# Kernel optimization log

Hardware: AMD Instinct MI355X
Metric: run time of the kernel (lower is better)

The kernel has to match this reference:

```python
import jax, jax.numpy as jnp
import numpy as np

B = 16          # graphs per batch
NN = 2000       # nodes per graph (num_nodes)
N = B * NN      # total nodes in the batched graph
F_IN = 128      # input node features
H, C = 4, 64    # heads, per-head out channels (both GAT layers)
HC = H * C
DEG = 12        # average degree per node
FC1, FC2, OUT = 512, 128, 1
FC_IN = 6 * NN  # len(which_layer) = 6


def setup_inputs() -> dict:
    key = jax.random.key(0)
    ks = jax.random.split(key, 32)

    def g(i, shape, s=0.05):
        return jax.random.normal(ks[i], shape, jnp.float32) * s

    # within-graph random edges, no self loops (GATConv removes then re-adds them)
    src_l = jax.random.randint(ks[0], (B, NN * DEG), 0, NN)
    off = jax.random.randint(ks[1], (B, NN * DEG), 1, NN)
    dst_l = (src_l + off) % NN
    goff = (jnp.arange(B) * NN)[:, None]
    edge_index = jnp.stack([(src_l + goff).reshape(-1),
                            (dst_l + goff).reshape(-1)]).astype(jnp.int32)

    return {
        "x": g(2, (N, F_IN), 1.0),
        "W1": g(3, (F_IN, HC)), "att_src1": g(4, (H, C)), "att_dst1": g(5, (H, C)),
        "b1": jnp.zeros((HC,), jnp.float32),
        "W2": g(6, (HC, HC)), "att_src2": g(7, (H, C)), "att_dst2": g(8, (H, C)),
        "b2": jnp.zeros((HC,), jnp.float32),
        "pw1": g(9, (HC, 1)), "pb1": jnp.zeros((1,), jnp.float32),
        "pw2": g(10, (HC, 1)), "pb2": jnp.zeros((1,), jnp.float32),
        "ln_w": jnp.ones((NN,), jnp.float32), "ln_b": jnp.zeros((NN,), jnp.float32),
        "sex_emb": g(11, (2, NN)), "mut_emb": g(12, (4, NN)),
        "age_w": g(13, (NN,)), "age_b": jnp.zeros((NN,), jnp.float32),
        "fw1": g(14, (FC_IN, FC1)), "fb1": jnp.zeros((FC1,), jnp.float32),
        "fw2": g(15, (FC1, FC2)), "fb2": jnp.zeros((FC2,), jnp.float32),
        "fw3": g(16, (FC2, OUT)), "fb3": jnp.zeros((OUT,), jnp.float32),
        "age": jax.random.uniform(ks[17], (B,), jnp.float32),
        "edge_index": edge_index,
        "sex": jax.random.randint(ks[18], (B,), 0, 2),
        "mutation": jax.random.randint(ks[19], (B,), 0, 4),
    }


def _layer_norm(x, w, b, eps=1e-5):
    mu = jnp.mean(x, -1, keepdims=True)
    var = jnp.mean((x - mu) ** 2, -1, keepdims=True)
    return (x - mu) / jnp.sqrt(var + eps) * w + b


def _gat_conv(x, W, att_src, att_dst, bias, src, dst):
    h = (x @ W).reshape(N, H, C)                         # [N,H,C]
    a_s = jnp.sum(h * att_src[None], -1)                 # [N,H]
    a_d = jnp.sum(h * att_dst[None], -1)                 # [N,H]
    alpha = jax.nn.leaky_relu(a_s[src] + a_d[dst], 0.2)  # [E,H]
    m = jax.ops.segment_max(alpha, dst, num_segments=N)  # segment softmax over dst
    e = jnp.exp(alpha - m[dst])
    denom = jax.ops.segment_sum(e, dst, num_segments=N)
    a = e / (denom[dst] + 1e-16)
    out = jax.ops.segment_sum(a[:, :, None] * h[src], dst, num_segments=N)
    return out.reshape(N, HC) + bias


def _forward(x, W1, att_src1, att_dst1, b1, W2, att_src2, att_dst2, b2,
             pw1, pb1, pw2, pb2, ln_w, ln_b, sex_emb, mut_emb, age_w, age_b,
             fw1, fb1, fw2, fb2, fw3, fb3, age, edge_index, sex, mutation):
    loop = jnp.arange(N, dtype=edge_index.dtype)         # self loops added by GATConv
    src = jnp.concatenate([edge_index[0], loop])
    dst = jnp.concatenate([edge_index[1], loop])

    x0 = jnp.mean(x, -1).reshape(B, NN)                  # to_dense_batch(mean(x,-1))

    h = jax.nn.relu(_gat_conv(x, W1, att_src1, att_dst1, b1, src, dst))
    x1 = (h @ pw1 + pb1).squeeze(-1).reshape(B, NN)
    h = jax.nn.relu(_gat_conv(h, W2, att_src2, att_dst2, b2, src, dst))
    x2 = (h @ pw2 + pb2).squeeze(-1).reshape(B, NN)

    x0 = _layer_norm(x0, ln_w, ln_b)
    x1 = _layer_norm(x1, ln_w, ln_b)
    x2 = _layer_norm(x2, ln_w, ln_b)
    ms = jnp.concatenate([x0, x1, x2], axis=1)           # [B, 3*NN]

    demo = jnp.concatenate([sex_emb[sex], mut_emb[mutation],
                            age[:, None] * age_w[None, :] + age_b], axis=1)
    t = jnp.concatenate([demo, ms], axis=1)              # [B, 6*NN]
    t = jax.nn.relu(t @ fw1 + fb1)
    t = jax.nn.relu(t @ fw2 + fb2)
    pred = t @ fw3 + fb3                                 # [B, 1]
    return pred, x0, x1, x2, ms


def reference(x, W1, att_src1, att_dst1, b1, W2, att_src2, att_dst2, b2,
              pw1, pb1, pw2, pb2, ln_w, ln_b, sex_emb, mut_emb, age_w, age_b,
              fw1, fb1, fw2, fb2, fw3, fb3, age, edge_index, sex, mutation):
    return _forward(x, W1, att_src1, att_dst1, b1, W2, att_src2, att_dst2, b2,
                    pw1, pb1, pw2, pb2, ln_w, ln_b, sex_emb, mut_emb, age_w, age_b,
                    fw1, fb1, fw2, fb2, fw3, fb3, age, edge_index, sex, mutation)
```

## Files before the change

kernel.cpp:

```cpp
#include <hip/hip_runtime.h>
#include <math.h>

#define NTOT   32000
#define NNODE  2000
#define NB     16
#define FIN    128
#define HCDIM  256
#define NH     4
#define FC1DIM 512
#define FC2DIM 128
#define FCIN   12000
#define NCH    125
#define KCC    96
#define CAP    64
#define BK     32
#define LPITCH 40
#define TRB    384
#define DEMOB  375

typedef __attribute__((ext_vector_type(8))) short bf16x8;
typedef __attribute__((ext_vector_type(4))) float f32x4;

__device__ inline float4 ld4(const float* p){ return *reinterpret_cast<const float4*>(p); }
__device__ inline void st4(float* p, float4 v){ *reinterpret_cast<float4*>(p) = v; }
__device__ inline float4 add4(float4 a, float4 b){ return make_float4(a.x+b.x,a.y+b.y,a.z+b.z,a.w+b.w); }
__device__ inline float lrelu(float x){ return x > 0.f ? x : 0.2f*x; }
__device__ inline float4 leaky4(float4 a){ return make_float4(lrelu(a.x),lrelu(a.y),lrelu(a.z),lrelu(a.w)); }
__device__ inline float4 exp4u(float4 a){ return make_float4(__expf(a.x),__expf(a.y),__expf(a.z),__expf(a.w)); }
__device__ inline float dot4(float4 a, float4 b){ return a.x*b.x + a.y*b.y + a.z*b.z + a.w*b.w; }
__device__ inline float selh(float4 v, int h){ return h==0 ? v.x : (h==1 ? v.y : (h==2 ? v.z : v.w)); }

__device__ inline unsigned short f2bf(float f){
  unsigned int u = __float_as_uint(f);
  u += 0x7FFFu + ((u >> 16) & 1u);
  return (unsigned short)(u >> 16);
}
__device__ inline unsigned int pk2bf(float a, float b){
  return (unsigned int)f2bf(a) | ((unsigned int)f2bf(b) << 16);
}
__device__ inline float bf2f(unsigned short h){
  return __uint_as_float(((unsigned int)h) << 16);
}
__device__ inline float4 ldbf4(const unsigned short* p){
  ushort4 v = *reinterpret_cast<const ushort4*>(p);
  return make_float4(bf2f(v.x), bf2f(v.y), bf2f(v.z), bf2f(v.w));
}

__global__ __launch_bounds__(256) void k_zero(int* __restrict__ cnt){
  int i = blockIdx.x*256 + threadIdx.x;
  if(i < NTOT) cnt[i] = 0;
}

__device__ __forceinline__ void ln_impl(const float* __restrict__ src,
                                        const float* __restrict__ lnw,
                                        const float* __restrict__ lnb,
                                        float* __restrict__ o1,
                                        float* __restrict__ o2,
                                        float* __restrict__ o3,
                                        float* red){
  int tid = threadIdx.x, lane = tid & 63, wv = tid >> 6;
  float s = 0.f, ss = 0.f;
  for(int i = tid; i < NNODE; i += 256){ float v = src[i]; s += v; ss += v*v; }
  #pragma unroll
  for(int off=1; off<64; off<<=1){ s += __shfl_xor(s, off); ss += __shfl_xor(ss, off); }
  if(lane == 0){ red[wv] = s; red[4+wv] = ss; }
  __syncthreads();
  s  = red[0]+red[1]+red[2]+red[3];
  ss = red[4]+red[5]+red[6]+red[7];
  float mu  = s * (1.0f/NNODE);
  float var = ss * (1.0f/NNODE) - mu*mu;
  float inv = 1.0f / sqrtf(var + 1e-5f);
  for(int i = tid; i < NNODE; i += 256){
    float v = (src[i]-mu)*inv*lnw[i] + lnb[i];
    o1[i] = v; o2[i] = v; o3[i] = v;
  }
}

__global__ void k_misc(const int* __restrict__ src, const int* __restrict__ dst,
                       int* __restrict__ cnt, int* __restrict__ col, int e0, int eb,
                       const float* __restrict__ W1, const float* __restrict__ W2,
                       unsigned short* __restrict__ W1t, unsigned short* __restrict__ W2t,
                       const float* __restrict__ sexemb, const float* __restrict__ mutemb,
                       const float* __restrict__ agew, const float* __restrict__ ageb,
                       const float* __restrict__ age, const int* __restrict__ sex,
                       const int* __restrict__ mut, float* __restrict__ t,
                       const float* __restrict__ x, float* __restrict__ x0r){
  int blk = blockIdx.x;
  if(blk < eb){
    int i = blk*256 + threadIdx.x;
    if(i < e0){
      int d = dst[i];
      int slot = atomicAdd(&cnt[d], 1);
      if(slot < CAP) col[(d<<6) + slot] = src[i];
    }
  } else if(blk < eb + TRB){
    int idx = (blk - eb)*256 + threadIdx.x;
    if(idx < HCDIM*FIN){
      int n = idx / FIN, k = idx - n*FIN;
      W1t[idx] = f2bf(W1[(size_t)k*HCDIM + n]);
    } else {
      int j = idx - HCDIM*FIN;
      int n = j / HCDIM, k = j - n*HCDIM;
      W2t[j] = f2bf(W2[(size_t)k*HCDIM + n]);
    }
  } else if(blk < eb + TRB + DEMOB){
    int i = (blk - eb - TRB)*256 + threadIdx.x;
    int b = i / (3*NNODE);
    int j = i - b*(3*NNODE);
    float v;
    if(j < NNODE)          v = sexemb[sex[b]*NNODE + j];
    else if(j < 2*NNODE)   v = mutemb[mut[b]*NNODE + (j - NNODE)];
    else                   v = age[b]*agew[j - 2*NNODE] + ageb[j - 2*NNODE];
    t[b*FCIN + j] = v;
  } else {
    int lane = threadIdx.x & 63, wv = threadIdx.x >> 6;
    int n = (blk - eb - TRB - DEMOB)*4 + wv;
    const float* r = x + (size_t)n*FIN;
    float2 v = *reinterpret_cast<const float2*>(r + lane*2);
    float s = v.x + v.y;
    #pragma unroll
    for(int off=1; off<64; off<<=1) s += __shfl_xor(s, off);
    if(lane == 0) x0r[n] = s * (1.0f/FIN);
  }
}

template<int AF32>
__global__ __launch_bounds__(256) void k_gemm_bf(const void* __restrict__ Av,
                                                 const unsigned short* __restrict__ Bt,
                                                 unsigned short* __restrict__ C,
                                                 const float* __restrict__ attS,
                                                 const float* __restrict__ attD,
                                                 float* __restrict__ a_s,
                                                 float* __restrict__ a_d,
                                                 int M, int K){
  const unsigned short* A = (const unsigned short*)Av;
  const float*         Af = (const float*)Av;
  __shared__ unsigned short As[128][LPITCH];
  __shared__ unsigned short Bs[128][LPITCH];
  int tid = threadIdx.x;
  int lane = tid & 63, wv = tid >> 6;
  int wm = (wv & 1)*64, wn = (wv >> 1)*64;
  int m0 = blockIdx.y*128, n0 = blockIdx.x*128;
  int l15 = lane & 15, lq = lane >> 4;
  f32x4 acc[4][4];
  #pragma unroll
  for(int i=0;i<4;i++)
    #pragma unroll
    for(int j=0;j<4;j++)
      acc[i][j] = (f32x4){0.f,0.f,0.f,0.f};

  int r = tid >> 2, c = (tid & 3)*8;
  for(int k0 = 0; k0 < K; k0 += BK){
    if(AF32){
      const float* pa  = Af + (size_t)(m0+r)*K + k0 + c;
      const float* pa2 = Af + (size_t)(m0+r+64)*K + k0 + c;
      float4 u0 = ld4(pa),  u1 = ld4(pa+4);
      float4 v0 = ld4(pa2), v1 = ld4(pa2+4);
      uint4 w0, w1;
      w0.x = pk2bf(u0.x,u0.y); w0.y = pk2bf(u0.z,u0.w);
      w0.z = pk2bf(u1.x,u1.y); w0.w = pk2bf(u1.z,u1.w);
      w1.x = pk2bf(v0.x,v0.y); w1.y = pk2bf(v0.z,v0.w);
      w1.z = pk2bf(v1.x,v1.y); w1.w = pk2bf(v1.z,v1.w);
      *reinterpret_cast<uint4*>(&As[r][c])    = w0;
      *reinterpret_cast<uint4*>(&As[r+64][c]) = w1;
    } else {
      *reinterpret_cast<uint4*>(&As[r][c])    = *reinterpret_cast<const uint4*>(A  + (size_t)(m0+r)*K + k0 + c);
      *reinterpret_cast<uint4*>(&As[r+64][c]) = *reinterpret_cast<const uint4*>(A  + (size_t)(m0+r+64)*K + k0 + c);
    }
    *reinterpret_cast<uint4*>(&Bs[r][c])    = *reinterpret_cast<const uint4*>(Bt + (size_t)(n0+r)*K + k0 + c);
    *reinterpret_cast<uint4*>(&Bs[r+64][c]) = *reinterpret_cast<const uint4*>(Bt + (size_t)(n0+r+64)*K + k0 + c);
    __syncthreads();
    bf16x8 af[4], bfr[4];
    #pragma unroll
    for(int i=0;i<4;i++){
      af[i]  = *reinterpret_cast<const bf16x8*>(&As[wm + i*16 + l15][lq*8]);
      bfr[i] = *reinterpret_cast<const bf16x8*>(&Bs[wn + i*16 + l15][lq*8]);
    }
    #pragma unroll
    for(int mi=0;mi<4;mi++)
      #pragma unroll
      for(int ni=0;ni<4;ni++)
        acc[mi][ni] = __builtin_amdgcn_mfma_f32_16x16x32_bf16(af[mi], bfr[ni], acc[mi][ni], 0, 0, 0);
    __syncthreads();
  }
  #pragma unroll
  for(int mi=0;mi<4;mi++){
    #pragma unroll
    for(int ni=0;ni<4;ni++){
      int cn = n0 + wn + ni*16 + l15;
      #pragma unroll
      for(int rg=0;rg<4;rg++){
        int rm = m0 + wm + mi*16 + lq*4 + rg;
        C[(size_t)rm*HCDIM + cn] = f2bf(acc[mi][ni][rg]);
      }
    }
  }
  int head = (n0 + wn) >> 6;
  float avs[4], avd[4];
  #pragma unroll
  for(int ni=0;ni<4;ni++){
    int cc = ni*16 + l15;
    avs[ni] = attS[head*64 + cc];
    avd[ni] = attD[head*64 + cc];
  }
  #pragma unroll
  for(int mi=0;mi<4;mi++){
    #pragma unroll
    for(int rg=0;rg<4;rg++){
      float ps = 0.f, pd = 0.f;
      #pragma unroll
      for(int ni=0;ni<4;ni++){
        float v = acc[mi][ni][rg];
        ps = fmaf(avs[ni], v, ps);
        pd = fmaf(avd[ni], v, pd);
      }
      #pragma unroll
      for(int off=1; off<16; off<<=1){
        ps += __shfl_xor(ps, off);
        pd += __shfl_xor(pd, off);
      }
      if(l15 == 0){
        int rm = m0 + wm + mi*16 + lq*4 + rg;
        a_s[rm*4 + head] = ps;
        a_d[rm*4 + head] = pd;
      }
    }
  }
}

template<int STORE>
__global__ __launch_bounds__(256) void k_agg(const unsigned short* __restrict__ hpre,
                                             const float* __restrict__ a_s,
                                             const float* __restrict__ a_d,
                                             const int* __restrict__ cnt,
                                             const int* __restrict__ col,
                                             const float* __restrict__ bias,
                                             const float* __restrict__ pw,
                                             const float* __restrict__ pb,
                                             unsigned short* __restrict__ hout,
                                             float* __restrict__ xraw,
                                             const float* __restrict__ lnsrc,
                                             const float* __restrict__ lnw,
                                             const float* __restrict__ lnb,
                                             float* __restrict__ out,
                                             float* __restrict__ t,
                                             int which){
  __shared__ float4 ew[4][CAP];
  __shared__ int    cols[4][CAP];
  __shared__ float  lred[8];
  int bx = blockIdx.x;
  if(bx < 16){
    int b = bx;
    ln_impl(lnsrc + b*NNODE, lnw, lnb,
            out + 16 + which*(NB*NNODE) + b*NNODE,
            out + 16 + 3*(NB*NNODE) + b*(3*NNODE) + which*NNODE,
            t + b*FCIN + 3*NNODE + which*NNODE, lred);
    return;
  }
  int tid = threadIdx.x;
  int lane = tid & 63, wv = tid >> 6;
  int blk  = bx - 16;
  int xcd  = blk & 7;
  int slot = blk >> 3;
  int half = slot / 500;
  int g    = xcd + 8*half;
  int n    = g*NNODE + (slot - half*500)*4 + wv;
  int f0 = lane*4;
  int hl = lane >> 4;
  float4 ad   = ld4(a_d + n*4);
  float4 asn  = ld4(a_s + n*4);
  float4 eself = exp4u(leaky4(add4(asn, ad)));
  int deg = min(cnt[n], CAP);
  int base = n << 6;
  if(lane < deg){
    int s = col[base + lane];
    cols[wv][lane] = s;
    ew[wv][lane] = exp4u(leaky4(add4(ld4(a_s + s*4), ad)));
  }
  float es = selh(eself, hl);
  float dsum = es;
  float4 hv = ldbf4(hpre + (size_t)n*HCDIM + f0);
  float4 acc = make_float4(es*hv.x, es*hv.y, es*hv.z, es*hv.w);
  const float* ewf = (const float*)&ew[wv][0];
  const int*   cwf = &cols[wv][0];
  for(int e = 0; e < deg; e++){
    int s = cwf[e];
    float w = ewf[e*4 + hl];
    dsum += w;
    float4 h2 = ldbf4(hpre + (size_t)s*HCDIM + f0);
    acc.x = fmaf(w, h2.x, acc.x); acc.y = fmaf(w, h2.y, acc.y);
    acc.z = fmaf(w, h2.z, acc.z); acc.w = fmaf(w, h2.w, acc.w);
  }
  float invh = 1.0f / (dsum + 1e-16f);
  float4 b4 = ld4(bias + f0);
  acc = make_float4(fmaxf(fmaf(acc.x,invh,b4.x),0.f), fmaxf(fmaf(acc.y,invh,b4.y),0.f),
                    fmaxf(fmaf(acc.z,invh,b4.z),0.f), fmaxf(fmaf(acc.w,invh,b4.w),0.f));
  if(STORE){
    ushort4 hb = make_ushort4(f2bf(acc.x), f2bf(acc.y), f2bf(acc.z), f2bf(acc.w));
    *reinterpret_cast<ushort4*>(hout + (size_t)n*HCDIM + f0) = hb;
  }
  float part = dot4(acc, ld4(pw + f0));
  #pragma unroll
  for(int off=1; off<64; off<<=1) part += __shfl_xor(part, off);
  if(lane == 0) xraw[n] = part + pb[0];
}

__global__ __launch_bounds__(256) void k_lnx2(const float* __restrict__ x2r,
                                              const float* __restrict__ lnw,
                                              const float* __restrict__ lnb,
                                              float* __restrict__ out,
                                              float* __restrict__ t){
  __shared__ float red[8];
  int b = blockIdx.x;
  ln_impl(x2r + b*NNODE, lnw, lnb,
          out + 16 + 2*(NB*NNODE) + b*NNODE,
          out + 16 + 3*(NB*NNODE) + b*(3*NNODE) + 2*NNODE,
          t + b*FCIN + 3*NNODE + 2*NNODE, red);
}

__global__ __launch_bounds__(256) void k_fc1(const float* __restrict__ t,
                                             const float* __restrict__ fw1,
                                             float* __restrict__ partial){
  __shared__ float ts[NB][KCC];
  int blk = blockIdx.x;
  int chunk = blk >> 1;
  int halfc = blk & 1;
  int tid = threadIdx.x;
  int k0 = chunk * KCC;
  #pragma unroll
  for(int i = tid; i < NB*KCC; i += 256){
    int b = i / KCC, kk = i - b*KCC;
    ts[b][kk] = t[b*FCIN + k0 + kk];
  }
  __syncthreads();
  int j = halfc*256 + tid;
  float acc[NB];
  #pragma unroll
  for(int b=0;b<NB;b++) acc[b] = 0.f;
  const float* wp = fw1 + (size_t)k0*FC1DIM + j;
  #pragma unroll 4
  for(int kk = 0; kk < KCC; kk++){
    float w = wp[(size_t)kk*FC1DIM];
    #pragma unroll
    for(int b=0;b<NB;b++) acc[b] = fmaf(ts[b][kk], w, acc[b]);
  }
  float* po = partial + (size_t)chunk*(NB*FC1DIM) + j;
  #pragma unroll
  for(int b=0;b<NB;b++) po[b*FC1DIM] = acc[b];
}

__global__ __launch_bounds__(256) void k_head(const float* __restrict__ partial,
                                              const float* __restrict__ fb1,
                                              const float* __restrict__ fw2,
                                              const float* __restrict__ fb2,
                                              const float* __restrict__ fw3,
                                              const float* __restrict__ fb3,
                                              float* __restrict__ pred){
  __shared__ float t1s[FC1DIM];
  __shared__ float red[2];
  int b = blockIdx.x, tid = threadIdx.x;
  int e1 = tid, e2 = tid + 256;
  float s1 = fb1[e1], s2 = fb1[e2];
  const float* pb_ = partial + (size_t)b*FC1DIM;
  for(int c = 0; c < NCH; c++){
    const float* pc = pb_ + (size_t)c*(NB*FC1DIM);
    s1 += pc[e1];
    s2 += pc[e2];
  }
  t1s[e1] = fmaxf(s1, 0.f);
  t1s[e2] = fmaxf(s2, 0.f);
  __syncthreads();
  if(tid < FC2DIM){
    int j = tid;
    float s = fb2[j];
    for(int k = 0; k < FC1DIM; k++) s = fmaf(t1s[k], fw2[k*FC2DIM + j], s);
    s = fmaxf(s, 0.f) * fw3[j];
    #pragma unroll
    for(int off=1; off<64; off<<=1) s += __shfl_xor(s, off);
    int lane = j & 63, wv = j >> 6;
    if(lane == 0) red[wv] = s;
  }
  __syncthreads();
  if(tid == 0) pred[b] = red[0] + red[1] + fb3[0];
}

extern "C" void kernel_launch(void* const* d_in, const int* in_sizes, int n_in,
                              void* d_out, int out_size, void* d_ws, size_t ws_size,
                              hipStream_t stream) {
  const float* x       = (const float*)d_in[0];
  const float* W1      = (const float*)d_in[1];
  const float* attS1   = (const float*)d_in[2];
  const float* attD1   = (const float*)d_in[3];
  const float* b1      = (const float*)d_in[4];
  const float* W2      = (const float*)d_in[5];
  const float* attS2   = (const float*)d_in[6];
  const float* attD2   = (const float*)d_in[7];
  const float* b2      = (const float*)d_in[8];
  const float* pw1     = (const float*)d_in[9];
  const float* pb1     = (const float*)d_in[10];
  const float* pw2     = (const float*)d_in[11];
  const float* pb2     = (const float*)d_in[12];
  const float* lnw     = (const float*)d_in[13];
  const float* lnb     = (const float*)d_in[14];
  const float* sexemb  = (const float*)d_in[15];
  const float* mutemb  = (const float*)d_in[16];
  const float* agew    = (const float*)d_in[17];
  const float* ageb    = (const float*)d_in[18];
  const float* fw1     = (const float*)d_in[19];
  const float* fb1     = (const float*)d_in[20];
  const float* fw2     = (const float*)d_in[21];
  const float* fb2     = (const float*)d_in[22];
  const float* fw3     = (const float*)d_in[23];
  const float* fb3     = (const float*)d_in[24];
  const float* age     = (const float*)d_in[25];
  const int*   eidx    = (const int*)d_in[26];
  const int*   sex     = (const int*)d_in[27];
  const int*   mut     = (const int*)d_in[28];
  const int E0 = in_sizes[26] / 2;
  const int* esrc = eidx;
  const int* edst = eidx + E0;

  float* out = (float*)d_out;

  float* w = (float*)d_ws;
  float* a_s  = w;
  float* a_d  = a_s + NTOT*NH;
  float* x0r  = a_d + NTOT*NH;
  float* x1r  = x0r + NTOT;
  float* x2r  = x1r + NTOT;
  float* tbuf = x2r + NTOT;
  float* part = tbuf + NB*FCIN;
  float* t1   = part + (size_t)240*NB*FC1DIM;
  unsigned short* hA  = (unsigned short*)(t1 + NB*FC1DIM);
  unsigned short* hB  = hA  + (size_t)NTOT*HCDIM;
  unsigned short* W1t = hB  + (size_t)NTOT*HCDIM;
  unsigned short* W2t = W1t + HCDIM*FIN;
  int* cnt    = (int*)(W2t + HCDIM*HCDIM);
  int* col    = cnt + NTOT;
  (void)ws_size; (void)n_in; (void)out_size;

  const int eb = (E0 + 255)/256;

  k_zero<<<(NTOT+255)/256, 256, 0, stream>>>(cnt);
  k_misc<<<eb + TRB + DEMOB + NTOT/4, 256, 0, stream>>>(esrc, edst, cnt, col, E0, eb,
                                               W1, W2, W1t, W2t,
                                               sexemb, mutemb, agew, ageb,
                                               age, sex, mut, tbuf, x, x0r);

  k_gemm_bf<1><<<dim3(HCDIM/128, NTOT/128), 256, 0, stream>>>(x, W1t, hA, attS1, attD1, a_s, a_d, NTOT, FIN);
  k_agg<1><<<16 + NTOT/4, 256, 0, stream>>>(hA, a_s, a_d, cnt, col, b1, pw1, pb1, hB, x1r,
                                            x0r, lnw, lnb, out, tbuf, 0);

  k_gemm_bf<0><<<dim3(HCDIM/128, NTOT/128), 256, 0, stream>>>(hB, W2t, hA, attS2, attD2, a_s, a_d, NTOT, HCDIM);
  k_agg<0><<<16 + NTOT/4, 256, 0, stream>>>(hA, a_s, a_d, cnt, col, b2, pw2, pb2, hB, x2r,
                                            x1r, lnw, lnb, out, tbuf, 1);

  k_lnx2<<<NB, 256, 0, stream>>>(x2r, lnw, lnb, out, tbuf);

  k_fc1<<<NCH*2, 256, 0, stream>>>(tbuf, fw1, part);
  k_head<<<NB, 256, 0, stream>>>(part, fb1, fw2, fb2, fw3, fb3, out);
}
```

Before: 276.3 us.

## Fuse x0 row-mean into GEMM, tile weight transpose, prefetch agg gathers, split FC

Moves the per-node input mean computation into the first GEMM's A-tile load so x is read once, and removes those blocks from the misc kernel. Replaces the scalar strided weight transpose with LDS-tiled 64x64 transposes for coalesced access. In the aggregation loop, the next neighbour's feature row is prefetched one step ahead using a sentinel column. Doubles the FC1 chunk count with smaller chunks and splits the FC2 dot over all 256 threads in the head kernel. These trade extra partial buffers and registers for better parallelism and less memory latency.

```diff
diff --git a/kernel.cpp b/kernel.cpp
--- a/kernel.cpp
+++ b/kernel.cpp
@@ -10,12 +10,12 @@
 #define FC1DIM 512
 #define FC2DIM 128
 #define FCIN   12000
-#define NCH    125
-#define KCC    96
+#define NCH    250
+#define KCC    48
 #define CAP    64
 #define BK     32
 #define LPITCH 40
-#define TRB    384
+#define TRB2   24
 #define DEMOB  375
 
 typedef __attribute__((ext_vector_type(8))) short bf16x8;
@@ -83,8 +83,8 @@
                        const float* __restrict__ sexemb, const float* __restrict__ mutemb,
                        const float* __restrict__ agew, const float* __restrict__ ageb,
                        const float* __restrict__ age, const int* __restrict__ sex,
-                       const int* __restrict__ mut, float* __restrict__ t,
-                       const float* __restrict__ x, float* __restrict__ x0r){
+                       const int* __restrict__ mut, float* __restrict__ t){
+  __shared__ float tile[64][65];
   int blk = blockIdx.x;
   if(blk < eb){
     int i = blk*256 + threadIdx.x;
@@ -93,18 +93,41 @@
       int slot = atomicAdd(&cnt[d], 1);
       if(slot < CAP) col[(d<<6) + slot] = src[i];
     }
-  } else if(blk < eb + TRB){
-    int idx = (blk - eb)*256 + threadIdx.x;
-    if(idx < HCDIM*FIN){
-      int n = idx / FIN, k = idx - n*FIN;
-      W1t[idx] = f2bf(W1[(size_t)k*HCDIM + n]);
+  } else if(blk < eb + TRB2){
+    int tb = blk - eb;
+    int wv = threadIdx.x >> 6, lane = threadIdx.x & 63;
+    if(tb < 8){
+      int tk = tb >> 2, tn = tb & 3;
+      int k0 = tk*64, n0 = tn*64;
+      #pragma unroll
+      for(int q=0;q<16;q++){
+        int row = q*4 + wv;
+        tile[row][lane] = W1[(size_t)(k0+row)*HCDIM + n0 + lane];
+      }
+      __syncthreads();
+      #pragma unroll
+      for(int q=0;q<16;q++){
+        int row = q*4 + wv;
+        W1t[(size_t)(n0+row)*FIN + k0 + lane] = f2bf(tile[lane][row]);
+      }
     } else {
-      int j = idx - HCDIM*FIN;
-      int n = j / HCDIM, k = j - n*HCDIM;
-      W2t[j] = f2bf(W2[(size_t)k*HCDIM + n]);
-    }
-  } else if(blk < eb + TRB + DEMOB){
-    int i = (blk - eb - TRB)*256 + threadIdx.x;
+      int t2 = tb - 8;
+      int tk = t2 >> 2, tn = t2 & 3;
+      int k0 = tk*64, n0 = tn*64;
+      #pragma unroll
+      for(int q=0;q<16;q++){
+        int row = q*4 + wv;
+        tile[row][lane] = W2[(size_t)(k0+row)*HCDIM + n0 + lane];
+      }
+      __syncthreads();
+      #pragma unroll
+      for(int q=0;q<16;q++){
+        int row = q*4 + wv;
+        W2t[(size_t)(n0+row)*HCDIM + k0 + lane] = f2bf(tile[lane][row]);
+      }
+    }
+  } else {
+    int i = (blk - eb - TRB2)*256 + threadIdx.x;
     int b = i / (3*NNODE);
     int j = i - b*(3*NNODE);
     float v;
@@ -112,15 +135,6 @@
     else if(j < 2*NNODE)   v = mutemb[mut[b]*NNODE + (j - NNODE)];
     else                   v = age[b]*agew[j - 2*NNODE] + ageb[j - 2*NNODE];
     t[b*FCIN + j] = v;
-  } else {
-    int lane = threadIdx.x & 63, wv = threadIdx.x >> 6;
-    int n = (blk - eb - TRB - DEMOB)*4 + wv;
-    const float* r = x + (size_t)n*FIN;
-    float2 v = *reinterpret_cast<const float2*>(r + lane*2);
-    float s = v.x + v.y;
-    #pragma unroll
-    for(int off=1; off<64; off<<=1) s += __shfl_xor(s, off);
-    if(lane == 0) x0r[n] = s * (1.0f/FIN);
   }
 }
 
@@ -132,6 +146,7 @@
                                                  const float* __restrict__ attD,
                                                  float* __restrict__ a_s,
                                                  float* __restrict__ a_d,
+                                                 float* __restrict__ x0r,
                                                  int M, int K){
   const unsigned short* A = (const unsigned short*)Av;
   const float*         Af = (const float*)Av;
@@ -150,12 +165,15 @@
       acc[i][j] = (f32x4){0.f,0.f,0.f,0.f};
 
   int r = tid >> 2, c = (tid & 3)*8;
+  float rs1 = 0.f, rs2 = 0.f;
   for(int k0 = 0; k0 < K; k0 += BK){
     if(AF32){
       const float* pa  = Af + (size_t)(m0+r)*K + k0 + c;
       const float* pa2 = Af + (size_t)(m0+r+64)*K + k0 + c;
       float4 u0 = ld4(pa),  u1 = ld4(pa+4);
       float4 v0 = ld4(pa2), v1 = ld4(pa2+4);
+      rs1 += (u0.x+u0.y+u0.z+u0.w) + (u1.x+u1.y+u1.z+u1.w);
+      rs2 += (v0.x+v0.y+v0.z+v0.w) + (v1.x+v1.y+v1.z+v1.w);
       uint4 w0, w1;
       w0.x = pk2bf(u0.x,u0.y); w0.y = pk2bf(u0.z,u0.w);
       w0.z = pk2bf(u1.x,u1.y); w0.w = pk2bf(u1.z,u1.w);
@@ -182,6 +200,15 @@
       for(int ni=0;ni<4;ni++)
         acc[mi][ni] = __builtin_amdgcn_mfma_f32_16x16x32_bf16(af[mi], bfr[ni], acc[mi][ni], 0, 0, 0);
     __syncthreads();
+  }
+  if(AF32 && n0 == 0){
+    float s1 = rs1, s2 = rs2;
+    s1 += __shfl_xor(s1,1); s1 += __shfl_xor(s1,2);
+    s2 += __shfl_xor(s2,1); s2 += __shfl_xor(s2,2);
+    if((tid & 3) == 0){
+      x0r[m0 + r]      = s1 * (1.0f/FIN);
+      x0r[m0 + r + 64] = s2 * (1.0f/FIN);
+    }
   }
   #pragma unroll
   for(int mi=0;mi<4;mi++){
@@ -246,7 +273,7 @@
                                              float* __restrict__ t,
                                              int which){
   __shared__ float4 ew[4][CAP];
-  __shared__ int    cols[4][CAP];
+  __shared__ int    cols[4][CAP+1];
   __shared__ float  lred[8];
   int bx = blockIdx.x;
   if(bx < 16){
@@ -276,20 +303,25 @@
     int s = col[base + lane];
     cols[wv][lane] = s;
     ew[wv][lane] = exp4u(leaky4(add4(ld4(a_s + s*4), ad)));
-  }
+  } else {
+    cols[wv][lane] = n;
+  }
+  if(lane == 0) cols[wv][CAP] = n;
   float es = selh(eself, hl);
   float dsum = es;
   float4 hv = ldbf4(hpre + (size_t)n*HCDIM + f0);
   float4 acc = make_float4(es*hv.x, es*hv.y, es*hv.z, es*hv.w);
   const float* ewf = (const float*)&ew[wv][0];
   const int*   cwf = &cols[wv][0];
+  float4 h2 = ldbf4(hpre + (size_t)cwf[0]*HCDIM + f0);
   for(int e = 0; e < deg; e++){
-    int s = cwf[e];
+    int sn = cwf[e+1];
+    float4 hn = ldbf4(hpre + (size_t)sn*HCDIM + f0);
     float w = ewf[e*4 + hl];
     dsum += w;
-    float4 h2 = ldbf4(hpre + (size_t)s*HCDIM + f0);
     acc.x = fmaf(w, h2.x, acc.x); acc.y = fmaf(w, h2.y, acc.y);
     acc.z = fmaf(w, h2.z, acc.z); acc.w = fmaf(w, h2.w, acc.w);
+    h2 = hn;
   }
   float invh = 1.0f / (dsum + 1e-16f);
   float4 b4 = ld4(bias + f0);
@@ -327,7 +359,6 @@
   int halfc = blk & 1;
   int tid = threadIdx.x;
   int k0 = chunk * KCC;
-  #pragma unroll
   for(int i = tid; i < NB*KCC; i += 256){
     int b = i / KCC, kk = i - b*KCC;
     ts[b][kk] = t[b*FCIN + k0 + kk];
@@ -338,7 +369,7 @@
   #pragma unroll
   for(int b=0;b<NB;b++) acc[b] = 0.f;
   const float* wp = fw1 + (size_t)k0*FC1DIM + j;
-  #pragma unroll 4
+  #pragma unroll 8
   for(int kk = 0; kk < KCC; kk++){
     float w = wp[(size_t)kk*FC1DIM];
     #pragma unroll
@@ -357,11 +388,13 @@
                                               const float* __restrict__ fb3,
                                               float* __restrict__ pred){
   __shared__ float t1s[FC1DIM];
+  __shared__ float ph[128];
   __shared__ float red[2];
   int b = blockIdx.x, tid = threadIdx.x;
   int e1 = tid, e2 = tid + 256;
   float s1 = fb1[e1], s2 = fb1[e2];
   const float* pb_ = partial + (size_t)b*FC1DIM;
+  #pragma unroll 4
   for(int c = 0; c < NCH; c++){
     const float* pc = pb_ + (size_t)c*(NB*FC1DIM);
     s1 += pc[e1];
@@ -370,15 +403,20 @@
   t1s[e1] = fmaxf(s1, 0.f);
   t1s[e2] = fmaxf(s2, 0.f);
   __syncthreads();
-  if(tid < FC2DIM){
-    int j = tid;
-    float s = fb2[j];
-    for(int k = 0; k < FC1DIM; k++) s = fmaf(t1s[k], fw2[k*FC2DIM + j], s);
+  int j = tid & 127, hc = tid >> 7;
+  float s = (hc == 0) ? fb2[j] : 0.f;
+  const float* w2 = fw2 + (size_t)(hc*256)*FC2DIM + j;
+  #pragma unroll 4
+  for(int k = 0; k < 256; k++) s = fmaf(t1s[hc*256 + k], w2[(size_t)k*FC2DIM], s);
+  if(hc == 1) ph[j] = s;
+  __syncthreads();
+  if(hc == 0){
+    s += ph[j];
     s = fmaxf(s, 0.f) * fw3[j];
     #pragma unroll
     for(int off=1; off<64; off<<=1) s += __shfl_xor(s, off);
-    int lane = j & 63, wv = j >> 6;
-    if(lane == 0) red[wv] = s;
+    int lane = j & 63, wv2 = j >> 6;
+    if(lane == 0) red[wv2] = s;
   }
   __syncthreads();
   if(tid == 0) pred[b] = red[0] + red[1] + fb3[0];
@@ -430,7 +468,7 @@
   float* x2r  = x1r + NTOT;
   float* tbuf = x2r + NTOT;
   float* part = tbuf + NB*FCIN;
-  float* t1   = part + (size_t)240*NB*FC1DIM;
+  float* t1   = part + (size_t)256*NB*FC1DIM;
   unsigned short* hA  = (unsigned short*)(t1 + NB*FC1DIM);
   unsigned short* hB  = hA  + (size_t)NTOT*HCDIM;
   unsigned short* W1t = hB  + (size_t)NTOT*HCDIM;
@@ -442,16 +480,16 @@
   const int eb = (E0 + 255)/256;
 
   k_zero<<<(NTOT+255)/256, 256, 0, stream>>>(cnt);
-  k_misc<<<eb + TRB + DEMOB + NTOT/4, 256, 0, stream>>>(esrc, edst, cnt, col, E0, eb,
+  k_misc<<<eb + TRB2 + DEMOB, 256, 0, stream>>>(esrc, edst, cnt, col, E0, eb,
                                                W1, W2, W1t, W2t,
                                                sexemb, mutemb, agew, ageb,
-                                               age, sex, mut, tbuf, x, x0r);
-
-  k_gemm_bf<1><<<dim3(HCDIM/128, NTOT/128), 256, 0, stream>>>(x, W1t, hA, attS1, attD1, a_s, a_d, NTOT, FIN);
+                                               age, sex, mut, tbuf);
+
+  k_gemm_bf<1><<<dim3(HCDIM/128, NTOT/128), 256, 0, stream>>>(x, W1t, hA, attS1, attD1, a_s, a_d, x0r, NTOT, FIN);
   k_agg<1><<<16 + NTOT/4, 256, 0, stream>>>(hA, a_s, a_d, cnt, col, b1, pw1, pb1, hB, x1r,
                                             x0r, lnw, lnb, out, tbuf, 0);
 
-  k_gemm_bf<0><<<dim3(HCDIM/128, NTOT/128), 256, 0, stream>>>(hB, W2t, hA, attS2, attD2, a_s, a_d, NTOT, HCDIM);
+  k_gemm_bf<0><<<dim3(HCDIM/128, NTOT/128), 256, 0, stream>>>(hB, W2t, hA, attS2, attD2, a_s, a_d, (float*)0, NTOT, HCDIM);
   k_agg<0><<<16 + NTOT/4, 256, 0, stream>>>(hA, a_s, a_d, cnt, col, b2, pw2, pb2, hB, x2r,
                                             x1r, lnw, lnb, out, tbuf, 1);
 
```

New measurement: 301.3 us. +9.1%, slower.
